# Kernel optimization log

Hardware: AMD Instinct MI355X
Metric: run time of the kernel (lower is better)

## Reference

```python
import jax, jax.numpy as jnp
import numpy as np

B, T, D, N, MW, WEMB = 1, 4096, 1024, 8192, 30, 20


def setup_inputs() -> dict:
    key = jax.random.key(0)
    k0, k1, k2, k3, k4 = jax.random.split(key, 5)
    inputs = jax.random.normal(k0, (B, T, D), dtype=jnp.float32)
    b = jax.random.randint(k1, (B, N), 0, T - MW)
    width = jax.random.randint(k2, (B, N), 0, MW)
    e = b + width  # e in [b, b+MW), always < T
    # learned params (std=0.02 init as in module)
    embed_w = (jax.random.normal(k3, (MW, WEMB), dtype=jnp.float32) * 0.02)
    attn_w = (jax.random.normal(k4, (D, 1), dtype=jnp.float32) * 0.02)
    attn_b = jnp.zeros((1,), dtype=jnp.float32)
    return {"inputs": inputs, "b": b, "e": e, "max_width": MW,
            "embed_w": embed_w, "attn_w": attn_w, "attn_b": attn_b}


def reference(inputs, b, e, max_width, embed_w, attn_w, attn_b):
    # inputs: [B,T,D], b/e: [B,N] int. Dropout is identity (eval mode).
    Bv, Tv, Dv = inputs.shape
    gather = jax.vmap(lambda x, idx: x[idx])  # [T,D],[N] -> [N,D]

    b_vec = gather(inputs, b)                                   # [B,N,D]
    e_vec = gather(inputs, jnp.minimum(e, Tv - 1))              # [B,N,D]

    width_idx = e - b                                           # [B,N]
    width_emb = embed_w[width_idx]                              # [B,N,WEMB]

    # attention-weighted head embedding (batch 0 only, as in original)
    token_attn = (inputs[0] @ attn_w)[:, 0] + attn_b[0]         # [T]
    tok = jnp.arange(Tv)
    span_mask = (tok[None, :] >= b[0][:, None]) & (tok[None, :] <= e[0][:, None])  # [N,T]
    # log(mask) + attn == where(mask, attn, -inf); each span has >=1 token
    attn = jax.nn.softmax(jnp.where(span_mask, token_attn[None, :], -jnp.inf), axis=1)
    head_emb = (attn @ inputs[0])[None]                         # [1,N,D]

    # masked span average
    w = jnp.arange(max_width)
    idxs = b[:, :, None] + w                                    # [B,N,W]
    span_toks = jax.vmap(lambda x, idx: x[idx])(inputs, jnp.minimum(idxs, Tv - 1))  # [B,N,W,D]
    m = (idxs <= e[:, :, None]).astype(inputs.dtype)            # [B,N,W]
    probs = m / m.sum(-1, keepdims=True)
    span_avg = jnp.einsum('bnw,bnwd->bnd', probs, span_toks)    # [B,N,D]

    vec = jnp.concatenate([b_vec, e_vec, width_emb, head_emb, span_avg], axis=-1)
    return vec, width_idx
```

## Files before the change

### kernel.cpp

```cpp
#include <hip/hip_runtime.h>
#include <math.h>

#define TT 4096
#define DD 1024
#define NSPAN 8192
#define MW 30
#define WEMB 20
#define VECW (4*DD + WEMB)

typedef float nf4 __attribute__((ext_vector_type(4)));

static __device__ __forceinline__ float dot4(const float4 a, const float4 b) {
    return fmaf(a.w, b.w, fmaf(a.z, b.z, fmaf(a.y, b.y, a.x * b.x)));
}
static __device__ __forceinline__ void fma4(float4& acc, const float w, const float4 v) {
    acc.x = fmaf(w, v.x, acc.x); acc.y = fmaf(w, v.y, acc.y);
    acc.z = fmaf(w, v.z, acc.z); acc.w = fmaf(w, v.w, acc.w);
}
static __device__ __forceinline__ void add4(float4& acc, const float4 v) {
    acc.x += v.x; acc.y += v.y; acc.z += v.z; acc.w += v.w;
}
static __device__ __forceinline__ void nstore(const float4 v, float* p) {
    nf4 t = { v.x, v.y, v.z, v.w };
    __builtin_nontemporal_store(t, (nf4*)p);
}

__global__ void __launch_bounds__(1024) sort_kernel(const int* __restrict__ bptr,
                                                    int* __restrict__ perm) {
    const int tid = threadIdx.x;
    __shared__ int h[TT];
    __shared__ int wsum[16];
    #pragma unroll
    for (int k = 0; k < 4; ++k) h[tid * 4 + k] = 0;
    __syncthreads();
    #pragma unroll
    for (int k = 0; k < NSPAN / 1024; ++k)
        atomicAdd(&h[bptr[k * 1024 + tid]], 1);
    __syncthreads();
    const int v0 = h[tid*4+0], v1 = h[tid*4+1], v2 = h[tid*4+2], v3 = h[tid*4+3];
    const int s = v0 + v1 + v2 + v3;
    const int lane = tid & 63;
    int incl = s;
    #pragma unroll
    for (int off = 1; off < 64; off <<= 1) {
        int t = __shfl_up(incl, off);
        if (lane >= off) incl += t;
    }
    if (lane == 63) wsum[tid >> 6] = incl;
    __syncthreads();
    if (tid < 16) {
        int ws = wsum[tid];
        #pragma unroll
        for (int off = 1; off < 16; off <<= 1) {
            int t = __shfl_up(ws, off);
            if (tid >= off) ws += t;
        }
        wsum[tid] = ws;
    }
    __syncthreads();
    const int waveoff = (tid >> 6) == 0 ? 0 : wsum[(tid >> 6) - 1];
    int excl = waveoff + (incl - s);
    h[tid*4+0] = excl;  excl += v0;
    h[tid*4+1] = excl;  excl += v1;
    h[tid*4+2] = excl;  excl += v2;
    h[tid*4+3] = excl;
    __syncthreads();
    #pragma unroll
    for (int k = 0; k < NSPAN / 1024; ++k) {
        const int n = k * 1024 + tid;
        const int pos = atomicAdd(&h[bptr[n]], 1);
        perm[pos] = n;
    }
}

#define PROC_ROW(C0, C1, C2, C3) do {                                        \
        float pd = (dot4(C0, w0) + dot4(C1, w1))                             \
                 + (dot4(C2, w2) + dot4(C3, w3));                            \
        pd += __shfl_xor(pd, 32); pd += __shfl_xor(pd, 16);                  \
        pd += __shfl_xor(pd, 8);  pd += __shfl_xor(pd, 4);                   \
        pd += __shfl_xor(pd, 2);  pd += __shfl_xor(pd, 1);                   \
        const float wg = exp2f(pd * 1.44269504f);                            \
        ssum += wg;                                                          \
        fma4(h0, wg, C0); fma4(h1, wg, C1); fma4(h2, wg, C2); fma4(h3, wg, C3); \
        add4(a0, C0); add4(a1, C1); add4(a2, C2); add4(a3, C3);              \
    } while (0)

__global__ void __launch_bounds__(256, 4) span_kernel(
        const float* __restrict__ x,
        const int* __restrict__ bptr,
        const int* __restrict__ eptr,
        const float* __restrict__ embed_w,
        const float* __restrict__ attn_w,
        const int* __restrict__ perm,
        float* __restrict__ out) {
    const int tid = threadIdx.x;
    const int wv  = tid >> 6;
    const int l   = tid & 63;
    const int blk  = (blockIdx.x & 7) * (NSPAN / 4 / 8) + (blockIdx.x >> 3);
    const int spos = blk * 4 + wv;
    const int n    = perm[spos];
    const int b     = bptr[n];
    const int e_raw = eptr[n];
    const int e     = min(e_raw, TT - 1);
    const int width = e_raw - b;
    const int len   = e - b + 1;

    const float4* aw = (const float4*)attn_w;
    const float4 w0 = aw[l], w1 = aw[64 + l], w2 = aw[128 + l], w3 = aw[192 + l];

    const float4* xr = (const float4*)(x + (size_t)b * DD);
    float* orow = out + (size_t)n * VECW;

    float4 c0 = xr[l], c1 = xr[64 + l], c2 = xr[128 + l], c3 = xr[192 + l];
    nstore(c0, orow + 4*l);
    nstore(c1, orow + 4*(64 + l));
    nstore(c2, orow + 4*(128 + l));
    nstore(c3, orow + 4*(192 + l));

    float  ssum = 0.0f;
    float4 h0 = {0,0,0,0}, h1 = {0,0,0,0}, h2 = {0,0,0,0}, h3 = {0,0,0,0};
    float4 a0 = {0,0,0,0}, a1 = {0,0,0,0}, a2 = {0,0,0,0}, a3 = {0,0,0,0};

    for (int i = 1; i < len; ++i) {
        const float4* row = xr + (size_t)i * 256;
        const float4 n0 = row[l], n1 = row[64 + l], n2 = row[128 + l], n3 = row[192 + l];
        PROC_ROW(c0, c1, c2, c3);
        c0 = n0; c1 = n1; c2 = n2; c3 = n3;
    }
    PROC_ROW(c0, c1, c2, c3);

    float* esec = orow + DD;
    nstore(c0, esec + 4*l);
    nstore(c1, esec + 4*(64 + l));
    nstore(c2, esec + 4*(128 + l));
    nstore(c3, esec + 4*(192 + l));

    const float invs = 1.0f / ssum;
    const float invl = 1.0f / (float)len;
    h0.x *= invs; h0.y *= invs; h0.z *= invs; h0.w *= invs;
    h1.x *= invs; h1.y *= invs; h1.z *= invs; h1.w *= invs;
    h2.x *= invs; h2.y *= invs; h2.z *= invs; h2.w *= invs;
    h3.x *= invs; h3.y *= invs; h3.z *= invs; h3.w *= invs;
    a0.x *= invl; a0.y *= invl; a0.z *= invl; a0.w *= invl;
    a1.x *= invl; a1.y *= invl; a1.z *= invl; a1.w *= invl;
    a2.x *= invl; a2.y *= invl; a2.z *= invl; a2.w *= invl;
    a3.x *= invl; a3.y *= invl; a3.z *= invl; a3.w *= invl;

    float* hsec = orow + 2*DD + WEMB;
    nstore(h0, hsec + 4*l);
    nstore(h1, hsec + 4*(64 + l));
    nstore(h2, hsec + 4*(128 + l));
    nstore(h3, hsec + 4*(192 + l));
    float* asec = orow + 3*DD + WEMB;
    nstore(a0, asec + 4*l);
    nstore(a1, asec + 4*(64 + l));
    nstore(a2, asec + 4*(128 + l));
    nstore(a3, asec + 4*(192 + l));

    if (l < 5) {
        const float4 we = ((const float4*)(embed_w + width * WEMB))[l];
        nstore(we, orow + 2*DD + 4*l);
    }
    if (l == 63)
        __builtin_nontemporal_store((float)width, out + (size_t)NSPAN * VECW + n);
}

extern "C" void kernel_launch(void* const* d_in, const int* in_sizes, int n_in,
                              void* d_out, int out_size, void* d_ws, size_t ws_size,
                              hipStream_t stream) {
    const float* x       = (const float*)d_in[0];
    const int*   b       = (const int*)  d_in[1];
    const int*   e       = (const int*)  d_in[2];
    const float* embed_w = (const float*)d_in[4];
    const float* attn_w  = (const float*)d_in[5];
    float* out = (float*)d_out;

    int* perm = (int*)d_ws;

    sort_kernel<<<1, 1024, 0, stream>>>(b, perm);
    span_kernel<<<NSPAN / 4, 256, 0, stream>>>(x, b, e, embed_w, attn_w, perm, out);
}
```

Before: 52.28 us.

## Precompute per-token attention logits once in prep kernel instead of per span row

Token attention scores are now computed once per token in a merged prep kernel (block 0 does the counting sort, other blocks compute the dot products with attn_w) and written to a workspace. The span kernel loads up to 30 precomputed logits per wave, exponentiates them in parallel across lanes, and broadcasts the weights with shuffles. This removes the per-row dot product and six-step shuffle reduction from the inner loop, which was recomputed redundantly for overlapping spans. In exchange it adds an extra read of all of x in the prep kernel and adds attn_b, which was previously ignored even though softmax cancels it.

```diff
diff --git a/kernel.cpp b/kernel.cpp
--- a/kernel.cpp
+++ b/kernel.cpp
@@ -10,9 +10,6 @@
 
 typedef float nf4 __attribute__((ext_vector_type(4)));
 
-static __device__ __forceinline__ float dot4(const float4 a, const float4 b) {
-    return fmaf(a.w, b.w, fmaf(a.z, b.z, fmaf(a.y, b.y, a.x * b.x)));
-}
 static __device__ __forceinline__ void fma4(float4& acc, const float w, const float4 v) {
     acc.x = fmaf(w, v.x, acc.x); acc.y = fmaf(w, v.y, acc.y);
     acc.z = fmaf(w, v.z, acc.z); acc.w = fmaf(w, v.w, acc.w);
@@ -25,72 +22,82 @@
     __builtin_nontemporal_store(t, (nf4*)p);
 }
 
-__global__ void __launch_bounds__(1024) sort_kernel(const int* __restrict__ bptr,
-                                                    int* __restrict__ perm) {
+__global__ void __launch_bounds__(1024) prep_kernel(
+        const float* __restrict__ x,
+        const float* __restrict__ attn_w,
+        const float* __restrict__ attn_b,
+        const int* __restrict__ bptr,
+        float* __restrict__ ta,
+        int* __restrict__ perm) {
     const int tid = threadIdx.x;
-    __shared__ int h[TT];
-    __shared__ int wsum[16];
-    #pragma unroll
-    for (int k = 0; k < 4; ++k) h[tid * 4 + k] = 0;
-    __syncthreads();
-    #pragma unroll
-    for (int k = 0; k < NSPAN / 1024; ++k)
-        atomicAdd(&h[bptr[k * 1024 + tid]], 1);
-    __syncthreads();
-    const int v0 = h[tid*4+0], v1 = h[tid*4+1], v2 = h[tid*4+2], v3 = h[tid*4+3];
-    const int s = v0 + v1 + v2 + v3;
-    const int lane = tid & 63;
-    int incl = s;
-    #pragma unroll
-    for (int off = 1; off < 64; off <<= 1) {
-        int t = __shfl_up(incl, off);
-        if (lane >= off) incl += t;
-    }
-    if (lane == 63) wsum[tid >> 6] = incl;
-    __syncthreads();
-    if (tid < 16) {
-        int ws = wsum[tid];
-        #pragma unroll
-        for (int off = 1; off < 16; off <<= 1) {
-            int t = __shfl_up(ws, off);
-            if (tid >= off) ws += t;
+    if (blockIdx.x == 0) {
+        __shared__ int h[TT];
+        __shared__ int wsum[16];
+        #pragma unroll
+        for (int k = 0; k < 4; ++k) h[tid * 4 + k] = 0;
+        __syncthreads();
+        #pragma unroll
+        for (int k = 0; k < NSPAN / 1024; ++k)
+            atomicAdd(&h[bptr[k * 1024 + tid]], 1);
+        __syncthreads();
+        const int v0 = h[tid*4+0], v1 = h[tid*4+1], v2 = h[tid*4+2], v3 = h[tid*4+3];
+        const int s = v0 + v1 + v2 + v3;
+        const int lane = tid & 63;
+        int incl = s;
+        #pragma unroll
+        for (int off = 1; off < 64; off <<= 1) {
+            int t = __shfl_up(incl, off);
+            if (lane >= off) incl += t;
         }
-        wsum[tid] = ws;
-    }
-    __syncthreads();
-    const int waveoff = (tid >> 6) == 0 ? 0 : wsum[(tid >> 6) - 1];
-    int excl = waveoff + (incl - s);
-    h[tid*4+0] = excl;  excl += v0;
-    h[tid*4+1] = excl;  excl += v1;
-    h[tid*4+2] = excl;  excl += v2;
-    h[tid*4+3] = excl;
-    __syncthreads();
-    #pragma unroll
-    for (int k = 0; k < NSPAN / 1024; ++k) {
-        const int n = k * 1024 + tid;
-        const int pos = atomicAdd(&h[bptr[n]], 1);
-        perm[pos] = n;
-    }
-}
-
-#define PROC_ROW(C0, C1, C2, C3) do {                                        \
-        float pd = (dot4(C0, w0) + dot4(C1, w1))                             \
-                 + (dot4(C2, w2) + dot4(C3, w3));                            \
-        pd += __shfl_xor(pd, 32); pd += __shfl_xor(pd, 16);                  \
-        pd += __shfl_xor(pd, 8);  pd += __shfl_xor(pd, 4);                   \
-        pd += __shfl_xor(pd, 2);  pd += __shfl_xor(pd, 1);                   \
-        const float wg = exp2f(pd * 1.44269504f);                            \
-        ssum += wg;                                                          \
-        fma4(h0, wg, C0); fma4(h1, wg, C1); fma4(h2, wg, C2); fma4(h3, wg, C3); \
-        add4(a0, C0); add4(a1, C1); add4(a2, C2); add4(a3, C3);              \
-    } while (0)
+        if (lane == 63) wsum[tid >> 6] = incl;
+        __syncthreads();
+        if (tid < 16) {
+            int ws = wsum[tid];
+            #pragma unroll
+            for (int off = 1; off < 16; off <<= 1) {
+                int t = __shfl_up(ws, off);
+                if (tid >= off) ws += t;
+            }
+            wsum[tid] = ws;
+        }
+        __syncthreads();
+        const int waveoff = (tid >> 6) == 0 ? 0 : wsum[(tid >> 6) - 1];
+        int excl = waveoff + (incl - s);
+        h[tid*4+0] = excl;  excl += v0;
+        h[tid*4+1] = excl;  excl += v1;
+        h[tid*4+2] = excl;  excl += v2;
+        h[tid*4+3] = excl;
+        __syncthreads();
+        #pragma unroll
+        for (int k = 0; k < NSPAN / 1024; ++k) {
+            const int n = k * 1024 + tid;
+            const int pos = atomicAdd(&h[bptr[n]], 1);
+            perm[pos] = n;
+        }
+    } else {
+        const int sub = tid >> 8;
+        const int l   = tid & 255;
+        const int t   = (blockIdx.x - 1) * 4 + sub;
+        const float4 v = ((const float4*)(x + (size_t)t * DD))[l];
+        const float4 w = ((const float4*)attn_w)[l];
+        float s = v.x * w.x + v.y * w.y + v.z * w.z + v.w * w.w;
+        #pragma unroll
+        for (int off = 32; off > 0; off >>= 1) s += __shfl_down(s, off);
+        __shared__ float part[16];
+        if ((tid & 63) == 0) part[tid >> 6] = s;
+        __syncthreads();
+        if (l == 0)
+            ta[t] = part[sub*4] + part[sub*4+1] + part[sub*4+2] + part[sub*4+3]
+                  + attn_b[0];
+    }
+}
 
 __global__ void __launch_bounds__(256, 4) span_kernel(
         const float* __restrict__ x,
         const int* __restrict__ bptr,
         const int* __restrict__ eptr,
         const float* __restrict__ embed_w,
-        const float* __restrict__ attn_w,
+        const float* __restrict__ ta,
         const int* __restrict__ perm,
         float* __restrict__ out) {
     const int tid = threadIdx.x;
@@ -105,8 +112,12 @@
     const int width = e_raw - b;
     const int len   = e - b + 1;
 
-    const float4* aw = (const float4*)attn_w;
-    const float4 w0 = aw[l], w1 = aw[64 + l], w2 = aw[128 + l], w3 = aw[192 + l];
+    float ex = 0.0f;
+    if (l < len) ex = exp2f(ta[b + l] * 1.44269504f);
+    float ssum = ex;
+    ssum += __shfl_xor(ssum, 32); ssum += __shfl_xor(ssum, 16);
+    ssum += __shfl_xor(ssum, 8);  ssum += __shfl_xor(ssum, 4);
+    ssum += __shfl_xor(ssum, 2);  ssum += __shfl_xor(ssum, 1);
 
     const float4* xr = (const float4*)(x + (size_t)b * DD);
     float* orow = out + (size_t)n * VECW;
@@ -117,17 +128,22 @@
     nstore(c2, orow + 4*(128 + l));
     nstore(c3, orow + 4*(192 + l));
 
-    float  ssum = 0.0f;
     float4 h0 = {0,0,0,0}, h1 = {0,0,0,0}, h2 = {0,0,0,0}, h3 = {0,0,0,0};
     float4 a0 = {0,0,0,0}, a1 = {0,0,0,0}, a2 = {0,0,0,0}, a3 = {0,0,0,0};
 
     for (int i = 1; i < len; ++i) {
         const float4* row = xr + (size_t)i * 256;
         const float4 n0 = row[l], n1 = row[64 + l], n2 = row[128 + l], n3 = row[192 + l];
-        PROC_ROW(c0, c1, c2, c3);
+        const float w = __shfl(ex, i - 1);
+        fma4(h0, w, c0); fma4(h1, w, c1); fma4(h2, w, c2); fma4(h3, w, c3);
+        add4(a0, c0); add4(a1, c1); add4(a2, c2); add4(a3, c3);
         c0 = n0; c1 = n1; c2 = n2; c3 = n3;
     }
-    PROC_ROW(c0, c1, c2, c3);
+    {
+        const float w = __shfl(ex, len - 1);
+        fma4(h0, w, c0); fma4(h1, w, c1); fma4(h2, w, c2); fma4(h3, w, c3);
+        add4(a0, c0); add4(a1, c1); add4(a2, c2); add4(a3, c3);
+    }
 
     float* esec = orow + DD;
     nstore(c0, esec + 4*l);
@@ -173,10 +189,12 @@
     const int*   e       = (const int*)  d_in[2];
     const float* embed_w = (const float*)d_in[4];
     const float* attn_w  = (const float*)d_in[5];
+    const float* attn_b  = (const float*)d_in[6];
     float* out = (float*)d_out;
 
-    int* perm = (int*)d_ws;
-
-    sort_kernel<<<1, 1024, 0, stream>>>(b, perm);
-    span_kernel<<<NSPAN / 4, 256, 0, stream>>>(x, b, e, embed_w, attn_w, perm, out);
-}
+    float* ta   = (float*)d_ws;
+    int*   perm = (int*)(ta + TT);
+
+    prep_kernel<<<1 + TT/4, 1024, 0, stream>>>(x, attn_w, attn_b, b, ta, perm);
+    span_kernel<<<NSPAN / 4, 256, 0, stream>>>(x, b, e, embed_w, ta, perm, out);
+}
```

Result: slower. 53.34 us (+2.0%).
